# Kernel tuning notes

Measured on AMD Instinct MI355X. Metric: run time of the kernel, lower is better.

Reference implementation:

```python
import jax, jax.numpy as jnp
import numpy as np

B, S, E, H = 4, 2048, 512, 8
D = E // H
DFF = 2048
EPS = 1e-5

def setup_inputs() -> dict:
    key = jax.random.key(0)
    ks = jax.random.split(key, 12)
    s = lambda fan: 1.0 / np.sqrt(fan)
    inp = {
        'x': jax.random.normal(ks[0], (B, S, E), dtype=jnp.float32),
        'dist': jax.random.uniform(ks[1], (B, S, S), dtype=jnp.float32),
        'mask': jnp.ones((B, S), dtype=jnp.int32),
        'Wq': jax.random.normal(ks[2], (E, E), dtype=jnp.float32) * s(E),
        'bq': jnp.zeros((E,), jnp.float32),
        'Wk': jax.random.normal(ks[3], (E, E), dtype=jnp.float32) * s(E),
        'bk': jnp.zeros((E,), jnp.float32),
        'Wv': jax.random.normal(ks[4], (E, E), dtype=jnp.float32) * s(E),
        'bv': jnp.zeros((E,), jnp.float32),
        'Wo': jax.random.normal(ks[5], (E, E), dtype=jnp.float32) * s(E),
        'bo': jnp.zeros((E,), jnp.float32),
        'W1': jax.random.normal(ks[6], (E, DFF), dtype=jnp.float32) * s(E),
        'b1': jnp.zeros((DFF,), jnp.float32),
        'W2': jax.random.normal(ks[7], (DFF, E), dtype=jnp.float32) * s(DFF),
        'b2': jnp.zeros((E,), jnp.float32),
        'g1': jnp.ones((E,), jnp.float32),
        'be1': jnp.zeros((E,), jnp.float32),
        'g2': jnp.ones((E,), jnp.float32),
        'be2': jnp.zeros((E,), jnp.float32),
    }
    return inp

def _layernorm(x, g, b):
    mu = jnp.mean(x, axis=-1, keepdims=True)
    var = jnp.mean(jnp.square(x - mu), axis=-1, keepdims=True)
    return (x - mu) * jax.lax.rsqrt(var + EPS) * g + b

def reference(x, dist, mask, Wq, bq, Wk, bk, Wv, bv, Wo, bo, W1, b1, W2, b2, g1, be1, g2, be2):
    b, s, e = x.shape
    split = lambda t: t.reshape(b, s, H, D).transpose(0, 2, 1, 3)  # [B,H,S,D]
    q = split(x @ Wq + bq)
    k = split(x @ Wk + bk)
    v = split(x @ Wv + bv)
    scale = D ** (-0.5)
    # scores: [B,H,S,S] with additive distance bias (0.4 * dist)
    scores = jnp.einsum('bhqd,bhkd->bhqk', q, k) * scale + 0.4 * dist[:, None, :, :]
    scores = jnp.where(mask[:, None, None, :] == 0, jnp.float32(-1e9), scores)
    w = jax.nn.softmax(scores, axis=-1)
    attn = jnp.einsum('bhqk,bhkd->bhqd', w, v).transpose(0, 2, 1, 3).reshape(b, s, e)
    attn_out = attn @ Wo + bo
    h = _layernorm(x + attn_out, g1, be1)
    ffn = jax.nn.relu(h @ W1 + b1) @ W2 + b2
    return _layernorm(h + ffn, g2, be2)
```

## Files before the change

### kernel.cpp

```cpp
#include <hip/hip_runtime.h>

#define B_ 4
#define S_ 2048
#define E_ 512
#define H_ 8
#define D_ 64
#define DFF_ 2048
#define M_ (B_*S_)

typedef unsigned short ushort_t;
typedef __bf16 bf16x8 __attribute__((ext_vector_type(8)));
typedef unsigned short u16x8 __attribute__((ext_vector_type(8)));
typedef unsigned short u16x4 __attribute__((ext_vector_type(4)));
typedef float f32x4 __attribute__((ext_vector_type(4)));

__device__ __forceinline__ unsigned short f2bf(float f){
  unsigned int u = __builtin_bit_cast(unsigned int, f);
  unsigned int r = (u + 0x7fffu + ((u >> 16) & 1u)) >> 16;
  return (unsigned short)r;
}
__device__ __forceinline__ float bf2f(unsigned short h){
  unsigned int u = ((unsigned int)h) << 16;
  return __builtin_bit_cast(float, u);
}
__device__ __forceinline__ unsigned pack_bf16x2(float a, float b){
  return (unsigned)f2bf(a) | ((unsigned)f2bf(b) << 16);
}

#define GLD_LDS16(g, l) __builtin_amdgcn_global_load_lds( \
    (const __attribute__((address_space(1))) void*)(g),   \
    (__attribute__((address_space(3))) void*)(l), 16, 0, 0)

#define MFMA16(a, b, c) __builtin_amdgcn_mfma_f32_16x16x32_bf16((a), (b), (c), 0, 0, 0)


__global__ __launch_bounds__(256)
void k_cast_x(const float* __restrict__ x, ushort_t* __restrict__ xb){
  const size_t i = ((size_t)blockIdx.x * 256 + threadIdx.x) * 8;
  float4 a = *(const float4*)(x + i);
  float4 c = *(const float4*)(x + i + 4);
  float y[8] = {a.x,a.y,a.z,a.w,c.x,c.y,c.z,c.w};
  u16x8 o;
  #pragma unroll
  for (int j = 0; j < 8; ++j) o[j] = f2bf(y[j]);
  *(u16x8*)(xb + i) = o;
}

__global__ __launch_bounds__(256)
void prep_dist(const float* __restrict__ dist, const int* __restrict__ mask,
               ushort_t* __restrict__ distb){
  const size_t flat = ((size_t)blockIdx.x * 256 + threadIdx.x) * 8;
  const int b = (int)(flat >> 22);
  const int rem = (int)(flat & 4194303u);
  const int k0 = rem & 2047;
  float4 a = *(const float4*)(dist + flat);
  float4 c = *(const float4*)(dist + flat + 4);
  const int4* mp = (const int4*)(mask + b*S_ + k0);
  int4 m0 = mp[0], m1 = mp[1];
  float y[8] = {a.x,a.y,a.z,a.w,c.x,c.y,c.z,c.w};
  int  mm[8] = {m0.x,m0.y,m0.z,m0.w,m1.x,m1.y,m1.z,m1.w};
  u16x8 o;
  #pragma unroll
  for (int i = 0; i < 8; ++i) o[i] = f2bf(mm[i] ? 0.4f*y[i] : -1e9f);
  *(u16x8*)(distb + flat) = o;
}

__global__ __launch_bounds__(256)
void k_transpose(const float* __restrict__ src, ushort_t* __restrict__ dst, int K, int N){
  __shared__ float t[32][33];
  const int nbn = N >> 5;
  const int bk = blockIdx.x / nbn, bn = blockIdx.x - bk * nbn;
  const int tx = threadIdx.x & 31, ty = threadIdx.x >> 5;
  #pragma unroll
  for (int p = 0; p < 4; ++p)
    t[ty + p*8][tx] = src[(size_t)(bk*32 + ty + p*8) * N + bn*32 + tx];
  __syncthreads();
  #pragma unroll
  for (int p = 0; p < 4; ++p)
    dst[(size_t)(bn*32 + ty + p*8) * K + bk*32 + tx] = f2bf(t[tx][ty + p*8]);
}

__global__ __launch_bounds__(256)
void k_bias3(const float* __restrict__ a, const float* __restrict__ b,
             const float* __restrict__ c, float* __restrict__ o){
  int i = blockIdx.x * 256 + threadIdx.x;
  if (i < 512) o[i] = a[i];
  else if (i < 1024) o[i] = b[i - 512];
  else if (i < 1536) o[i] = c[i - 1024];
}


template<int MODE>
__global__ __launch_bounds__(256)
void gemm_bt(const ushort_t* __restrict__ A, const ushort_t* __restrict__ Bt,
             const float* __restrict__ bias, const float* __restrict__ resid,
             void* __restrict__ out, int Md, int Nd, int Kd)
{
  __shared__ ushort_t sm[2][2][128*32];
  const int tid = threadIdx.x;
  const int lane = tid & 63, wid = tid >> 6;
  const int wr = wid >> 1, wc = wid & 1;
  const int nbn = Nd >> 7;
  const int bm = blockIdx.x / nbn;
  const int bn = blockIdx.x - bm * nbn;
  const int rq = lane & 15, kg = (lane >> 4) << 3;

  f32x4 acc[4][4];
  #pragma unroll
  for (int i = 0; i < 4; ++i)
    #pragma unroll
    for (int j = 0; j < 4; ++j) acc[i][j] = (f32x4){0.f,0.f,0.f,0.f};

  const int nkt = Kd >> 5;
  const int c0 = tid, c1 = tid + 256;
  const int rA0 = c0 >> 2, koA0 = (c0 & 3) << 3;
  const int rA1 = c1 >> 2, koA1 = (c1 & 3) << 3;
  const ushort_t* Abase = A + (size_t)(bm * 128) * Kd;
  const ushort_t* Bbase = Bt + (size_t)(bn * 128) * Kd;

  auto stage = [&](int buf, int kt){
    const int k0 = kt << 5;
    GLD_LDS16(Abase + (size_t)rA0 * Kd + k0 + koA0, &sm[buf][0][c0 * 8]);
    GLD_LDS16(Abase + (size_t)rA1 * Kd + k0 + koA1, &sm[buf][0][c1 * 8]);
    GLD_LDS16(Bbase + (size_t)rA0 * Kd + k0 + koA0, &sm[buf][1][c0 * 8]);
    GLD_LDS16(Bbase + (size_t)rA1 * Kd + k0 + koA1, &sm[buf][1][c1 * 8]);
  };

  stage(0, 0);
  __syncthreads();
  int cur = 0;
  for (int kt = 0; kt < nkt; ++kt){
    if (kt + 1 < nkt) stage(cur ^ 1, kt + 1);
    const ushort_t* As = &sm[cur][0][0];
    const ushort_t* Bs = &sm[cur][1][0];
    bf16x8 af[4], bfr[4];
    #pragma unroll
    for (int i = 0; i < 4; ++i) af[i]  = *(const bf16x8*)&As[(wr*64 + i*16 + rq)*32 + kg];
    #pragma unroll
    for (int j = 0; j < 4; ++j) bfr[j] = *(const bf16x8*)&Bs[(wc*64 + j*16 + rq)*32 + kg];
    #pragma unroll
    for (int i = 0; i < 4; ++i)
      #pragma unroll
      for (int j = 0; j < 4; ++j)
        acc[i][j] = MFMA16(af[i], bfr[j], acc[i][j]);
    __syncthreads();
    cur ^= 1;
  }

  const int rb = (lane >> 4) << 2;
  #pragma unroll
  for (int i = 0; i < 4; ++i){
    #pragma unroll
    for (int j = 0; j < 4; ++j){
      const int col = bn*128 + wc*64 + j*16 + rq;
      const float bs = bias[col];
      #pragma unroll
      for (int r = 0; r < 4; ++r){
        const int row = bm*128 + wr*64 + i*16 + rb + r;
        const float v = acc[i][j][r] + bs;
        if (MODE == 0){
          ushort_t* o = (ushort_t*)out;
          const int which = col >> 9, hd = col & 511;
          const int hh = hd >> 6, dd = hd & 63;
          const int bb = row >> 11, ss = row & 2047;
          o[(size_t)which*(B_*H_*S_*D_) + (((size_t)(bb*H_ + hh))*S_ + ss)*D_ + dd] = f2bf(v);
        } else if (MODE == 1){
          float* o = (float*)out;
          o[(size_t)row*Nd + col] = v + resid[(size_t)row*Nd + col];
        } else {
          ushort_t* o = (ushort_t*)out;
          o[(size_t)row*Nd + col] = f2bf(fmaxf(v, 0.f));
        }
      }
    }
  }
}


__global__ __launch_bounds__(256)
void attn_fused(const ushort_t* __restrict__ qkv,
                const ushort_t* __restrict__ distb,
                ushort_t* __restrict__ attnb)
{
  __shared__ ushort_t Ks [2][64*64];
  __shared__ ushort_t Vts[2][64*64];
  __shared__ ushort_t Ds [2][64*64];
  __shared__ ushort_t Ps [4][16*64];

  const int tid = threadIdx.x, lane = tid & 63, w = tid >> 6;
  const int blk = blockIdx.x;
  const int h = blk & 7, qt = (blk >> 3) & 31, b = blk >> 8;
  const size_t plane = (size_t)S_ * D_;
  const ushort_t* Q  = qkv + (size_t)(b*H_ + h) * plane;
  const ushort_t* Kg = Q + (size_t)B_*H_*plane;
  const ushort_t* Vg = Q + 2 * (size_t)B_*H_*plane;
  const ushort_t* distq = distb + (size_t)b * S_ * S_;

  const int rq = lane & 15, g = lane >> 4;
  const int q0b = qt * 64;
  const int q0 = q0b + w*16;
  const float LOG2E = 1.4426950408889634f;

  bf16x8 qf[2];
  #pragma unroll
  for (int kk = 0; kk < 2; ++kk)
    qf[kk] = *(const bf16x8*)&Q[(size_t)(q0 + rq)*D_ + kk*32 + g*8];

  f32x4 ao[4];
  #pragma unroll
  for (int j = 0; j < 4; ++j) ao[j] = (f32x4){0.f,0.f,0.f,0.f};
  float mi = -1e30f, li = 0.f;

  const int cK0 = tid, cK1 = tid + 256;
  auto stageK = [&](int buf, int kt){
    const char* Kt = (const char*)(Kg + (size_t)kt * 64 * D_);
    const int pb0 = cK0 * 16, pb1 = cK1 * 16;
    const int lb0 = pb0 ^ ((((unsigned)pb0 >> 7) & 7) << 4);
    const int lb1 = pb1 ^ ((((unsigned)pb1 >> 7) & 7) << 4);
    GLD_LDS16(Kt + lb0, (char*)&Ks[buf][0] + pb0);
    GLD_LDS16(Kt + lb1, (char*)&Ks[buf][0] + pb1);
  };
  auto stageD = [&](int buf, int kt){
    #pragma unroll
    for (int hh = 0; hh < 2; ++hh){
      const int pbd = (tid + hh*256) * 16;
      const int qrl = pbd >> 7;
      const int lbd = pbd ^ (((pbd >> 7) & 7) << 4);
      const char* src = (const char*)(distq + (size_t)(q0b + qrl) * S_ + kt*64) + (lbd & 127);
      GLD_LDS16(src, (char*)&Ds[buf][0] + pbd);
    }
  };
  auto loadV = [&](int kt, u16x8* vr){
    const ushort_t* Vt = Vg + (size_t)kt * 64 * D_;
    vr[0] = *(const u16x8*)&Vt[cK0 * 8];
    vr[1] = *(const u16x8*)&Vt[cK1 * 8];
  };
  auto writeV = [&](int buf, const u16x8* vr){
    #pragma unroll
    for (int hh = 0; hh < 2; ++hh){
      const int c = tid + hh * 256;
      const int key = c >> 3, d0 = (c & 7) << 3;
      #pragma unroll
      for (int i2 = 0; i2 < 8; ++i2){
        const int dd = d0 + i2;
        const int lb = dd * 128 + key * 2;
        const int pb = lb ^ ((dd & 7) << 4);
        *(ushort_t*)((char*)&Vts[buf][0] + pb) = vr[hh][i2];
      }
    }
  };

  u16x8 vr0[2];
  stageK(0, 0);
  stageD(0, 0);
  loadV(0, vr0);
  writeV(0, vr0);
  __syncthreads();

  int cur = 0;
  const int NT = S_ / 64;
  for (int kt = 0; kt < NT; ++kt){
    u16x8 vn[2];
    if (kt + 1 < NT){
      loadV(kt + 1, vn);
      stageK(cur ^ 1, kt + 1);
      stageD(cur ^ 1, kt + 1);
    }
    u16x4 dv[4];
    #pragma unroll
    for (int j = 0; j < 4; ++j){
      const int logical = (w*16 + rq)*128 + j*32 + g*8;
      const int phys = logical ^ ((rq & 7) << 4);
      dv[j] = *(const u16x4*)((const char*)&Ds[cur][0] + phys);
    }
    f32x4 sc[4];
    #pragma unroll
    for (int j = 0; j < 4; ++j) sc[j] = (f32x4){0.f,0.f,0.f,0.f};
    __builtin_amdgcn_s_setprio(1);
    #pragma unroll
    for (int kk = 0; kk < 2; ++kk){
      #pragma unroll
      for (int j = 0; j < 4; ++j){
        const int phys = ((j*16 + rq)*128 + kk*64 + g*16) ^ ((rq & 7) << 4);
        bf16x8 kf = *(const bf16x8*)((const char*)&Ks[cur][0] + phys);
        sc[j] = MFMA16(kf, qf[kk], sc[j]);
      }
    }
    __builtin_amdgcn_s_setprio(0);
    float sv[4][4];
    #pragma unroll
    for (int j = 0; j < 4; ++j)
      #pragma unroll
      for (int r = 0; r < 4; ++r)
        sv[j][r] = fmaf(sc[j][r], 0.125f, bf2f(dv[j][r]));
    float pm = sv[0][0];
    #pragma unroll
    for (int j = 0; j < 4; ++j)
      #pragma unroll
      for (int r = 0; r < 4; ++r) pm = fmaxf(pm, sv[j][r]);
    pm = fmaxf(pm, __shfl_xor(pm, 16));
    pm = fmaxf(pm, __shfl_xor(pm, 32));
    const int allskip = __all(pm <= mi + 8.f);
    if (!allskip){
      const float mn = fmaxf(mi, pm);
      const float corr = exp2f((mi - mn) * LOG2E);
      mi = mn;
      li *= corr;
      #pragma unroll
      for (int r = 0; r < 4; ++r){
        const int ci = __builtin_amdgcn_ds_bpermute((g*4 + r) << 2,
                         __builtin_bit_cast(int, corr));
        const float c4 = __builtin_bit_cast(float, ci);
        #pragma unroll
        for (int jd = 0; jd < 4; ++jd) ao[jd][r] *= c4;
      }
    }
    const float mL = mi * LOG2E;
    float p[4][4];
    float rs = 0.f;
    #pragma unroll
    for (int j = 0; j < 4; ++j)
      #pragma unroll
      for (int r = 0; r < 4; ++r){
        p[j][r] = exp2f(fmaf(sv[j][r], LOG2E, -mL));
        rs += p[j][r];
      }
    rs += __shfl_xor(rs, 16);
    rs += __shfl_xor(rs, 32);
    li += rs;
    #pragma unroll
    for (int j = 0; j < 4; ++j)
      #pragma unroll
      for (int t = 0; t < 2; ++t){
        const unsigned u = pack_bf16x2(p[j][2*t], p[j][2*t + 1]);
        const int logical = rq*128 + j*32 + g*8 + t*4;
        const int phys = logical ^ ((rq & 7) << 4);
        *(unsigned*)((char*)&Ps[w][0] + phys) = u;
      }
    asm volatile("s_waitcnt lgkmcnt(0)" ::: "memory");
    __builtin_amdgcn_sched_barrier(0);
    __builtin_amdgcn_s_setprio(1);
    #pragma unroll
    for (int kk = 0; kk < 2; ++kk){
      const int physp = (rq*128 + kk*64 + g*16) ^ ((rq & 7) << 4);
      bf16x8 pf = *(const bf16x8*)((const char*)&Ps[w][0] + physp);
      #pragma unroll
      for (int jd = 0; jd < 4; ++jd){
        const int drow = jd*16 + rq;
        const int physv = (drow*128 + kk*64 + g*16) ^ ((rq & 7) << 4);
        bf16x8 vf = *(const bf16x8*)((const char*)&Vts[cur][0] + physv);
        ao[jd] = MFMA16(pf, vf, ao[jd]);
      }
    }
    __builtin_amdgcn_s_setprio(0);
    if (kt + 1 < NT) writeV(cur ^ 1, vn);
    __syncthreads();
    cur ^= 1;
  }

  ushort_t* ob = attnb + (size_t)b * S_ * E_ + h * D_;
  float inv[4];
  #pragma unroll
  for (int r = 0; r < 4; ++r){
    const int li_i = __builtin_amdgcn_ds_bpermute((g*4 + r) << 2,
                       __builtin_bit_cast(int, li));
    inv[r] = 1.f / __builtin_bit_cast(float, li_i);
  }
  #pragma unroll
  for (int jd = 0; jd < 4; ++jd)
    #pragma unroll
    for (int r = 0; r < 4; ++r){
      const int qrow = q0 + g*4 + r;
      ob[(size_t)qrow * E_ + jd*16 + rq] = f2bf(ao[jd][r] * inv[r]);
    }
}


template<int WB>
__global__ __launch_bounds__(256)
void ln_kernel(const float* __restrict__ in, const float* __restrict__ gam,
               const float* __restrict__ bet, float* __restrict__ outf,
               ushort_t* __restrict__ outb)
{
  const int lane = threadIdx.x & 63;
  const size_t row = (size_t)blockIdx.x * 4 + (threadIdx.x >> 6);
  const float* xr = in + row * E_;
  const int e0 = lane * 8;
  float4 a = *(const float4*)(xr + e0);
  float4 c = *(const float4*)(xr + e0 + 4);
  float y[8] = {a.x,a.y,a.z,a.w,c.x,c.y,c.z,c.w};
  float s = 0.f, s2 = 0.f;
  #pragma unroll
  for (int i = 0; i < 8; ++i){ s += y[i]; s2 += y[i]*y[i]; }
  #pragma unroll
  for (int m = 1; m < 64; m <<= 1){ s += __shfl_xor(s, m); s2 += __shfl_xor(s2, m); }
  const float mu = s * (1.f / E_);
  const float rsd = rsqrtf(s2 * (1.f / E_) - mu*mu + 1e-5f);
  float4 G0 = *(const float4*)(gam + e0), G1 = *(const float4*)(gam + e0 + 4);
  float4 B0 = *(const float4*)(bet + e0), B1 = *(const float4*)(bet + e0 + 4);
  float gg[8] = {G0.x,G0.y,G0.z,G0.w,G1.x,G1.y,G1.z,G1.w};
  float bb[8] = {B0.x,B0.y,B0.z,B0.w,B1.x,B1.y,B1.z,B1.w};
  float o[8];
  #pragma unroll
  for (int i = 0; i < 8; ++i) o[i] = (y[i] - mu) * rsd * gg[i] + bb[i];
  float4 w0 = {o[0],o[1],o[2],o[3]}, w1 = {o[4],o[5],o[6],o[7]};
  *(float4*)(outf + row * E_ + e0) = w0;
  *(float4*)(outf + row * E_ + e0 + 4) = w1;
  if (WB){
    u16x8 ob;
    #pragma unroll
    for (int i = 0; i < 8; ++i) ob[i] = f2bf(o[i]);
    *(u16x8*)(outb + row * E_ + e0) = ob;
  }
}


extern "C" void kernel_launch(void* const* d_in, const int* in_sizes, int n_in,
                              void* d_out, int out_size, void* d_ws, size_t ws_size,
                              hipStream_t stream)
{
  const float* x    = (const float*)d_in[0];
  const float* dist = (const float*)d_in[1];
  const int*   mask = (const int*)d_in[2];
  const float* Wq = (const float*)d_in[3];  const float* bq = (const float*)d_in[4];
  const float* Wk = (const float*)d_in[5];  const float* bk = (const float*)d_in[6];
  const float* Wv = (const float*)d_in[7];  const float* bv = (const float*)d_in[8];
  const float* Wo = (const float*)d_in[9];  const float* bo = (const float*)d_in[10];
  const float* W1 = (const float*)d_in[11]; const float* b1 = (const float*)d_in[12];
  const float* W2 = (const float*)d_in[13]; const float* b2 = (const float*)d_in[14];
  const float* g1 = (const float*)d_in[15]; const float* be1 = (const float*)d_in[16];
  const float* g2 = (const float*)d_in[17]; const float* be2 = (const float*)d_in[18];
  float* out = (float*)d_out;

  char* ws = (char*)d_ws;
  ushort_t* xb    = (ushort_t*)(ws + 0);
  ushort_t* wtqkv = (ushort_t*)(ws + 8388608);
  ushort_t* wto   = (ushort_t*)(ws + 9961472);
  ushort_t* wt1   = (ushort_t*)(ws + 10485760);
  ushort_t* wt2   = (ushort_t*)(ws + 12582912);
  float*    bqkv  = (float*)(ws + 14680064);
  ushort_t* qkvb  = (ushort_t*)(ws + 14686208);
  ushort_t* attnb = (ushort_t*)(ws + 39852032);
  ushort_t* f1    = (ushort_t*)(ws + 14686208);
  ushort_t* distb = (ushort_t*)(ws + 48240640);
  float*    resid1= (float*)(ws + 48240640);
  float*    resid2= (float*)(ws + 48240640);
  float*    hf    = (float*)(ws + 65017856);
  ushort_t* hb    = (ushort_t*)(ws + 81795072);

  k_cast_x<<<2048, 256, 0, stream>>>(x, xb);
  prep_dist<<<8192, 256, 0, stream>>>(dist, mask, distb);
  k_transpose<<<16*16, 256, 0, stream>>>(Wq, wtqkv + 0,      512, 512);
  k_transpose<<<16*16, 256, 0, stream>>>(Wk, wtqkv + 262144, 512, 512);
  k_transpose<<<16*16, 256, 0, stream>>>(Wv, wtqkv + 524288, 512, 512);
  k_transpose<<<16*16, 256, 0, stream>>>(Wo, wto, 512, 512);
  k_transpose<<<16*64, 256, 0, stream>>>(W1, wt1, 512, 2048);
  k_transpose<<<64*16, 256, 0, stream>>>(W2, wt2, 2048, 512);
  k_bias3<<<6, 256, 0, stream>>>(bq, bk, bv, bqkv);

  gemm_bt<0><<<64*12, 256, 0, stream>>>(xb, wtqkv, bqkv, nullptr, qkvb, M_, 1536, 512);
  attn_fused<<<1024, 256, 0, stream>>>(qkvb, distb, attnb);
  gemm_bt<1><<<64*4, 256, 0, stream>>>(attnb, wto, bo, x, resid1, M_, 512, 512);
  ln_kernel<1><<<2048, 256, 0, stream>>>(resid1, g1, be1, hf, hb);
  gemm_bt<2><<<64*16, 256, 0, stream>>>(hb, wt1, b1, nullptr, f1, M_, 2048, 512);
  gemm_bt<1><<<64*4, 256, 0, stream>>>(f1, wt2, b2, hf, resid2, M_, 512, 2048);
  ln_kernel<0><<<2048, 256, 0, stream>>>(resid2, g2, be2, out, nullptr);
}
```

Before: 454.7 us.

## Load distance bias straight to registers and pack V transpose writes

The attention kernel no longer stages the distance tile through shared memory. Each lane now loads its own bias values from global memory into registers one tile ahead, which removes the Ds buffer and its LDS traffic. The V transpose is reorganized so each thread writes packed 32-bit pairs of keys instead of single 16-bit elements, and the P tile is stored with 64-bit writes. Launch bounds now request higher occupancy. The per-lane global bias loads are narrower and less coalesced, which risks more memory latency and higher register pressure.

```diff
diff --git a/kernel.cpp b/kernel.cpp
--- a/kernel.cpp
+++ b/kernel.cpp
@@ -12,6 +12,7 @@
 typedef __bf16 bf16x8 __attribute__((ext_vector_type(8)));
 typedef unsigned short u16x8 __attribute__((ext_vector_type(8)));
 typedef unsigned short u16x4 __attribute__((ext_vector_type(4)));
+typedef unsigned u32x2 __attribute__((ext_vector_type(2)));
 typedef float f32x4 __attribute__((ext_vector_type(4)));
 
 __device__ __forceinline__ unsigned short f2bf(float f){
@@ -177,14 +178,13 @@
 }
 
 
-__global__ __launch_bounds__(256)
+__global__ __launch_bounds__(256, 4)
 void attn_fused(const ushort_t* __restrict__ qkv,
                 const ushort_t* __restrict__ distb,
                 ushort_t* __restrict__ attnb)
 {
   __shared__ ushort_t Ks [2][64*64];
   __shared__ ushort_t Vts[2][64*64];
-  __shared__ ushort_t Ds [2][64*64];
   __shared__ ushort_t Ps [4][16*64];
 
   const int tid = threadIdx.x, lane = tid & 63, w = tid >> 6;
@@ -220,40 +220,34 @@
     GLD_LDS16(Kt + lb0, (char*)&Ks[buf][0] + pb0);
     GLD_LDS16(Kt + lb1, (char*)&Ks[buf][0] + pb1);
   };
-  auto stageD = [&](int buf, int kt){
-    #pragma unroll
-    for (int hh = 0; hh < 2; ++hh){
-      const int pbd = (tid + hh*256) * 16;
-      const int qrl = pbd >> 7;
-      const int lbd = pbd ^ (((pbd >> 7) & 7) << 4);
-      const char* src = (const char*)(distq + (size_t)(q0b + qrl) * S_ + kt*64) + (lbd & 127);
-      GLD_LDS16(src, (char*)&Ds[buf][0] + pbd);
-    }
-  };
+  const int kp = tid & 31, ds8 = tid >> 5;
   auto loadV = [&](int kt, u16x8* vr){
     const ushort_t* Vt = Vg + (size_t)kt * 64 * D_;
-    vr[0] = *(const u16x8*)&Vt[cK0 * 8];
-    vr[1] = *(const u16x8*)&Vt[cK1 * 8];
+    vr[0] = *(const u16x8*)&Vt[(2*kp)     * D_ + ds8*8];
+    vr[1] = *(const u16x8*)&Vt[(2*kp + 1) * D_ + ds8*8];
   };
   auto writeV = [&](int buf, const u16x8* vr){
     #pragma unroll
-    for (int hh = 0; hh < 2; ++hh){
-      const int c = tid + hh * 256;
-      const int key = c >> 3, d0 = (c & 7) << 3;
-      #pragma unroll
-      for (int i2 = 0; i2 < 8; ++i2){
-        const int dd = d0 + i2;
-        const int lb = dd * 128 + key * 2;
-        const int pb = lb ^ ((dd & 7) << 4);
-        *(ushort_t*)((char*)&Vts[buf][0] + pb) = vr[hh][i2];
-      }
+    for (int e = 0; e < 8; ++e){
+      const int d = ds8*8 + e;
+      const unsigned u = (unsigned)vr[0][e] | ((unsigned)vr[1][e] << 16);
+      const int lb = d*128 + kp*4;
+      const int pb = lb ^ ((d & 7) << 4);
+      *(unsigned*)((char*)&Vts[buf][0] + pb) = u;
     }
   };
+  auto loadD = [&](int kt, u16x4* dr){
+    const ushort_t* Dp = distq + (size_t)(q0 + rq) * S_ + kt*64;
+    #pragma unroll
+    for (int j = 0; j < 4; ++j)
+      dr[j] = *(const u16x4*)&Dp[j*16 + g*4];
+  };
 
   u16x8 vr0[2];
+  u16x4 dv[4], dvn[4];
   stageK(0, 0);
-  stageD(0, 0);
   loadV(0, vr0);
+  loadD(0, dv);
   writeV(0, vr0);
   __syncthreads();
 
@@ -264,14 +258,7 @@
     if (kt + 1 < NT){
       loadV(kt + 1, vn);
       stageK(cur ^ 1, kt + 1);
-      stageD(cur ^ 1, kt + 1);
-    }
-    u16x4 dv[4];
-    #pragma unroll
-    for (int j = 0; j < 4; ++j){
-      const int logical = (w*16 + rq)*128 + j*32 + g*8;
-      const int phys = logical ^ ((rq & 7) << 4);
-      dv[j] = *(const u16x4*)((const char*)&Ds[cur][0] + phys);
+      loadD(kt + 1, dvn);
     }
     f32x4 sc[4];
     #pragma unroll
@@ -329,14 +316,14 @@
     rs += __shfl_xor(rs, 32);
     li += rs;
     #pragma unroll
-    for (int j = 0; j < 4; ++j)
-      #pragma unroll
-      for (int t = 0; t < 2; ++t){
-        const unsigned u = pack_bf16x2(p[j][2*t], p[j][2*t + 1]);
-        const int logical = rq*128 + j*32 + g*8 + t*4;
-        const int phys = logical ^ ((rq & 7) << 4);
-        *(unsigned*)((char*)&Ps[w][0] + phys) = u;
-      }
+    for (int j = 0; j < 4; ++j){
+      u32x2 u;
+      u[0] = pack_bf16x2(p[j][0], p[j][1]);
+      u[1] = pack_bf16x2(p[j][2], p[j][3]);
+      const int logical = rq*128 + j*32 + g*8;
+      const int phys = logical ^ ((rq & 7) << 4);
+      *(u32x2*)((char*)&Ps[w][0] + phys) = u;
+    }
     asm volatile("s_waitcnt lgkmcnt(0)" ::: "memory");
     __builtin_amdgcn_sched_barrier(0);
     __builtin_amdgcn_s_setprio(1);
@@ -355,6 +342,8 @@
     __builtin_amdgcn_s_setprio(0);
     if (kt + 1 < NT) writeV(cur ^ 1, vn);
     __syncthreads();
+    #pragma unroll
+    for (int j = 0; j < 4; ++j) dv[j] = dvn[j];
     cur ^= 1;
   }
 
```

Result: faster. 406.0 us (-10.7%).
